# Optimization experiments

Hardware: AMD Instinct MI355X
Metric: run time of the kernel (lower is better)

## Reference

```python
import jax, jax.numpy as jnp
import numpy as np

N_NODES = 32768
N_EDGES = 131072
B = 1024          # number of drug graphs
N_SIDE = 994      # SIDER side effects
SIDE_F = 1050     # glove(300) + label(750)

GAT_DIMS = [(109, 96, 8), (768, 128, 8), (1024, 128, 8), (1024, 128, 1)]  # (in, out_per_head, heads)
LIN_DIMS = [("x5", 128, 64), ("x6", 64, 64), ("w1", 750, 750), ("w2", 750, 64),
            ("z1", 19127, 1600), ("z2", 1600, 64), ("v1", 1024, 256), ("v2", 256, 64),
            ("agg", 192, 64), ("col", 128, 64), ("s1", SIDE_F, 64), ("s2", 64, 64)]


def setup_inputs() -> dict:
    key = jax.random.key(0)
    ks = iter(jax.random.split(key, 64))
    d = {}
    d["x"] = jax.random.normal(next(ks), (N_NODES, 109), jnp.float32)
    d["edge_index"] = jax.random.randint(next(ks), (2, N_EDGES), 0, N_NODES)
    d["batch"] = jnp.arange(N_NODES) // (N_NODES // B)  # 32 atoms per graph
    d["w"] = jax.random.normal(next(ks), (B, 750), jnp.float32)
    d["z"] = jax.random.normal(next(ks), (B, 19127), jnp.float32)
    d["v"] = jax.random.normal(next(ks), (B, 1024), jnp.float32)
    d["side"] = jax.random.normal(next(ks), (N_SIDE, SIDE_F), jnp.float32)
    for i, (fi, fo, h) in enumerate(GAT_DIMS, 1):
        d[f"g{i}_W"] = jax.random.normal(next(ks), (fi, h * fo), jnp.float32) / np.sqrt(fi)
        d[f"g{i}_as"] = jax.random.normal(next(ks), (1, h, fo), jnp.float32) * 0.1
        d[f"g{i}_ad"] = jax.random.normal(next(ks), (1, h, fo), jnp.float32) * 0.1
        d[f"g{i}_b"] = jnp.zeros((h * fo,), jnp.float32)
    for name, fi, fo in LIN_DIMS:
        d[name + "_W"] = jax.random.normal(next(ks), (fi, fo), jnp.float32) / np.sqrt(fi)
        d[name + "_b"] = jnp.zeros((fo,), jnp.float32)
    return d


def _gat(x, src, dst, W, a_s, a_d, b, heads, ch):
    """PyG GATConv (eval mode): linear -> per-edge leaky_relu attention ->
    scatter-softmax over incoming edges (self-loops already in src/dst) -> scatter-sum."""
    N = x.shape[0]
    h = (x @ W).reshape(N, heads, ch)            # [N,H,C]
    al_s = (h * a_s).sum(-1)                     # [N,H]
    al_d = (h * a_d).sum(-1)                     # [N,H]
    e = jax.nn.leaky_relu(al_s[src] + al_d[dst], 0.2)  # [E,H]
    m = jax.ops.segment_max(e, dst, num_segments=N)
    p = jnp.exp(e - m[dst])
    s = jax.ops.segment_sum(p, dst, num_segments=N)
    alpha = p / s[dst]                           # softmax over neighbors of dst
    out = jax.ops.segment_sum(h[src] * alpha[:, :, None], dst, num_segments=N)
    return out.reshape(N, heads * ch) + b


def reference(x, edge_index, batch, w, z, v, side,
              g1_W, g1_as, g1_ad, g1_b, g2_W, g2_as, g2_ad, g2_b,
              g3_W, g3_as, g3_ad, g3_b, g4_W, g4_as, g4_ad, g4_b,
              x5_W, x5_b, x6_W, x6_b, w1_W, w1_b, w2_W, w2_b,
              z1_W, z1_b, z2_W, z2_b, v1_W, v1_b, v2_W, v2_b,
              agg_W, agg_b, col_W, col_b, s1_W, s1_b, s2_W, s2_b):
    relu = jax.nn.relu
    N = x.shape[0]
    nb = w.shape[0]
    loops = jnp.arange(N)
    src = jnp.concatenate([edge_index[0], loops])  # add_self_loops=True (PyG default)
    dst = jnp.concatenate([edge_index[1], loops])
    h = relu(_gat(x, src, dst, g1_W, g1_as, g1_ad, g1_b, 8, 96))
    h = relu(_gat(h, src, dst, g2_W, g2_as, g2_ad, g2_b, 8, 128))
    h = relu(_gat(h, src, dst, g3_W, g3_as, g3_ad, g3_b, 8, 128))
    h = relu(_gat(h, src, dst, g4_W, g4_as, g4_ad, g4_b, 1, 128))
    xg = jax.ops.segment_max(h, batch, num_segments=nb)           # global_max_pool
    xg = relu(relu(xg @ x5_W + x5_b) @ x6_W + x6_b)
    wv = relu(relu(w @ w1_W + w1_b) @ w2_W + w2_b)
    zv = relu(relu(z @ z1_W + z1_b) @ z2_W + z2_b)
    vv = relu(relu(v @ v1_W + v1_b) @ v2_W + v2_b)
    xwz = jnp.concatenate([xg, wv, zv], axis=1) @ agg_W + agg_b   # no activation
    drug = jnp.abs(jnp.tanh(jnp.concatenate([xwz, vv], axis=1) @ col_W + col_b))
    se = jnp.tanh(relu(side @ s1_W + s1_b) @ s2_W + s2_b)
    dn = drug / jnp.maximum(jnp.linalg.norm(drug, axis=1, keepdims=True), 1e-12)
    sn = se / jnp.maximum(jnp.linalg.norm(se, axis=1, keepdims=True), 1e-12)
    freq = 5.0 * (dn @ sn.T)
    return (freq, dn, sn)
```

## Files before the change

### kernel.cpp

```cpp
#include <hip/hip_runtime.h>
#include <math.h>
#include <float.h>

#define E0 131072
#define NN 32768
#define NB 1024
#define NSIDE 994
#define ETOT (E0 + NN)

typedef short bf16x8 __attribute__((ext_vector_type(8)));
typedef unsigned short ushort8 __attribute__((ext_vector_type(8)));
typedef float f32x4 __attribute__((ext_vector_type(4)));

__device__ inline float b2f(unsigned short u) { return __uint_as_float(((unsigned)u) << 16); }
__device__ inline unsigned short f2b(float f) {
  unsigned u = __float_as_uint(f);
  return (unsigned short)((u + 0x7fffu + ((u >> 16) & 1u)) >> 16);
}

__device__ inline void gload_lds16(const void* g, void* l) {
  __builtin_amdgcn_global_load_lds(
      (const __attribute__((address_space(1))) unsigned int*)g,
      (__attribute__((address_space(3))) unsigned int*)l, 16, 0, 0);
}

__global__ void fill_i32(int* p, int v, int n) {
  int i = blockIdx.x * blockDim.x + threadIdx.x;
  if (i < n) p[i] = v;
}

struct CDesc { const float* in; unsigned short* out; int rowsOut, Rreal, C, Cp, wg_end; };
struct CBatch { CDesc d[5]; };
__global__ void conv_batch(CBatch cb) {
  int bid = blockIdx.x;
  int di = 0;
  while (bid >= cb.d[di].wg_end) ++di;
  const CDesc& g = cb.d[di];
  int rel = bid - (di ? cb.d[di - 1].wg_end : 0);
  size_t idx = (size_t)rel * 256 + threadIdx.x;
  size_t tot = (size_t)g.rowsOut * g.Cp;
  if (idx >= tot) return;
  int r = (int)(idx / g.Cp), c = (int)(idx % g.Cp);
  g.out[idx] = (r < g.Rreal && c < g.C) ? f2b(g.in[(size_t)r * g.C + c]) : (unsigned short)0;
}

struct TDesc { const float* W; unsigned short* WT; int K, N, Kp, Npad, gx, wg_end; };
struct TBatch { TDesc d[16]; };
__global__ __launch_bounds__(256) void transpose_batch(TBatch tb) {
  __shared__ float t[32][33];
  int bid = blockIdx.x;
  int di = 0;
  while (bid >= tb.d[di].wg_end) ++di;
  const TDesc& g = tb.d[di];
  int rel = bid - (di ? tb.d[di - 1].wg_end : 0);
  int n0 = (rel % g.gx) * 32, k0 = (rel / g.gx) * 32;
  int tx = threadIdx.x & 31, ty = threadIdx.x >> 5;
  for (int r = ty; r < 32; r += 8) {
    int k = k0 + r, n = n0 + tx;
    t[r][tx] = (k < g.K && n < g.N) ? g.W[(size_t)k * g.N + n] : 0.f;
  }
  __syncthreads();
  for (int r = ty; r < 32; r += 8) {
    int n = n0 + r, k = k0 + tx;
    if (n < g.Npad && k < g.Kp)
      g.WT[(size_t)n * g.Kp + k] = (n < g.N) ? f2b(t[tx][r]) : (unsigned short)0;
  }
}

__global__ void count_deg(const int* __restrict__ ei, int* deg) {
  int e = blockIdx.x * blockDim.x + threadIdx.x;
  if (e >= ETOT) return;
  int dst = (e < E0) ? ei[E0 + e] : (e - E0);
  atomicAdd(&deg[dst], 1);
}

__global__ void scan_deg(const int* __restrict__ deg, int* rowptr, int* cursor) {
  __shared__ int part[1024];
  int tid = threadIdx.x;
  const int chunk = NN / 1024;
  int base = tid * chunk;
  int local[chunk];
  int sum = 0;
#pragma unroll
  for (int i = 0; i < chunk; ++i) { local[i] = sum; sum += deg[base + i]; }
  part[tid] = sum;
  __syncthreads();
  for (int off = 1; off < 1024; off <<= 1) {
    int t = (tid >= off) ? part[tid - off] : 0;
    __syncthreads();
    part[tid] += t;
    __syncthreads();
  }
  int offset = part[tid] - sum;
#pragma unroll
  for (int i = 0; i < chunk; ++i) {
    int v = offset + local[i];
    rowptr[base + i] = v;
    cursor[base + i] = v;
  }
  if (tid == 1023) rowptr[NN] = offset + sum;
}

__global__ void fill_csr(const int* __restrict__ ei, int* cursor,
                         int* __restrict__ srcl, int* __restrict__ pos) {
  int e = blockIdx.x * blockDim.x + threadIdx.x;
  if (e >= ETOT) return;
  int src, dst;
  if (e < E0) { src = ei[e]; dst = ei[E0 + e]; } else { src = dst = e - E0; }
  int p = atomicAdd(&cursor[dst], 1);
  srcl[p] = src;
  pos[e] = p;
}

template <int ACT, int OBF>
__global__ __launch_bounds__(256) void gemm_mfma(
    const unsigned short* __restrict__ A, const unsigned short* __restrict__ BT,
    const float* __restrict__ bias, void* __restrict__ Cp,
    int Nreal, int K, int lda, int ldb, int ldc, int gx, int zpad) {
  __shared__ unsigned short As[2][128 * 32];
  __shared__ unsigned short Bs[2][128 * 32];
  const int nwg = gridDim.x;
  const int chunk = nwg >> 3;
  const int bid = blockIdx.x;
  const int swz = (bid & 7) * chunk + (bid >> 3);
  const int bm = (swz / gx) * 128, bn = (swz % gx) * 128;
  const int tid = threadIdx.x;
  const int wv = tid >> 6, lane = tid & 63;
  const int sr = lane >> 2;
  const int sk = ((lane & 3) ^ ((lane >> 3) & 3)) * 8;
  const int r16 = lane & 15, kq = lane >> 4;
  const int slot8 = (kq ^ ((r16 >> 1) & 3)) * 8;
  const int wr = wv >> 1, wc = wv & 1;
  f32x4 acc[4][4];
#pragma unroll
  for (int i = 0; i < 4; ++i)
#pragma unroll
    for (int j = 0; j < 4; ++j) acc[i][j] = (f32x4){0.f, 0.f, 0.f, 0.f};

  const unsigned short* Abase = A + (size_t)bm * lda;
  const unsigned short* Bbase = BT + (size_t)bn * ldb;
  auto stage = [&](int buf, int k0) {
    gload_lds16(Abase + (size_t)(wv * 16 + sr) * lda + k0 + sk, &As[buf][wv * 512]);
    gload_lds16(Abase + (size_t)(64 + wv * 16 + sr) * lda + k0 + sk, &As[buf][2048 + wv * 512]);
    gload_lds16(Bbase + (size_t)(wv * 16 + sr) * ldb + k0 + sk, &Bs[buf][wv * 512]);
    gload_lds16(Bbase + (size_t)(64 + wv * 16 + sr) * ldb + k0 + sk, &Bs[buf][2048 + wv * 512]);
  };
  stage(0, 0);
  __syncthreads();
  int cur = 0;
  for (int k0 = 0; k0 < K; k0 += 32) {
    if (k0 + 32 < K) stage(cur ^ 1, k0 + 32);
    bf16x8 af[4], bfr[4];
#pragma unroll
    for (int i = 0; i < 4; ++i)
      af[i] = *(const bf16x8*)&As[cur][(wr * 64 + i * 16 + r16) * 32 + slot8];
#pragma unroll
    for (int j = 0; j < 4; ++j)
      bfr[j] = *(const bf16x8*)&Bs[cur][(wc * 64 + j * 16 + r16) * 32 + slot8];
#pragma unroll
    for (int i = 0; i < 4; ++i)
#pragma unroll
      for (int j = 0; j < 4; ++j)
        acc[i][j] = __builtin_amdgcn_mfma_f32_16x16x32_bf16(af[i], bfr[j], acc[i][j], 0, 0, 0);
    __syncthreads();
    cur ^= 1;
  }
#pragma unroll
  for (int i = 0; i < 4; ++i) {
    int row = bm + wr * 64 + i * 16 + kq * 4;
#pragma unroll
    for (int j = 0; j < 4; ++j) {
      int col = bn + wc * 64 + j * 16 + r16;
      bool real = col < Nreal;
      if (!real && !zpad) continue;
      float bv = (bias && real) ? bias[col] : 0.f;
#pragma unroll
      for (int r = 0; r < 4; ++r) {
        float v = acc[i][j][r] + bv;
        if (ACT == 1) v = v > 0.f ? v : 0.f;
        else if (ACT == 2) v = tanhf(v);
        else if (ACT == 3) v = fabsf(tanhf(v));
        if (!real) v = 0.f;
        if (OBF) ((unsigned short*)Cp)[(size_t)(row + r) * ldc + col] = f2b(v);
        else ((float*)Cp)[(size_t)(row + r) * ldc + col] = v;
      }
    }
  }
}

struct GDesc {
  const unsigned short* A; const unsigned short* BT; const float* bias; void* C;
  int Nreal, K, lda, ldb, ldc, gx, zpad, act, obf, Mreal, wg_end;
};
struct GBatch { GDesc d[5]; };
__global__ __launch_bounds__(256) void gemm_batch(GBatch gb) {
  __shared__ unsigned short As[2][128 * 32];
  __shared__ unsigned short Bs[2][128 * 32];
  int bid = blockIdx.x;
  int di = 0;
  while (bid >= gb.d[di].wg_end) ++di;
  const GDesc& g = gb.d[di];
  int rel = bid - (di ? gb.d[di - 1].wg_end : 0);
  const int bm = (rel / g.gx) * 128, bn = (rel % g.gx) * 128;
  const int tid = threadIdx.x;
  const int wv = tid >> 6, lane = tid & 63;
  const int sr = lane >> 2;
  const int sk = ((lane & 3) ^ ((lane >> 3) & 3)) * 8;
  const int r16 = lane & 15, kq = lane >> 4;
  const int slot8 = (kq ^ ((r16 >> 1) & 3)) * 8;
  const int wr = wv >> 1, wc = wv & 1;
  f32x4 acc[4][4];
#pragma unroll
  for (int i = 0; i < 4; ++i)
#pragma unroll
    for (int j = 0; j < 4; ++j) acc[i][j] = (f32x4){0.f, 0.f, 0.f, 0.f};

  const unsigned short* Abase = g.A + (size_t)bm * g.lda;
  const unsigned short* Bbase = g.BT + (size_t)bn * g.ldb;
  auto stage = [&](int buf, int k0) {
    gload_lds16(Abase + (size_t)(wv * 16 + sr) * g.lda + k0 + sk, &As[buf][wv * 512]);
    gload_lds16(Abase + (size_t)(64 + wv * 16 + sr) * g.lda + k0 + sk, &As[buf][2048 + wv * 512]);
    gload_lds16(Bbase + (size_t)(wv * 16 + sr) * g.ldb + k0 + sk, &Bs[buf][wv * 512]);
    gload_lds16(Bbase + (size_t)(64 + wv * 16 + sr) * g.ldb + k0 + sk, &Bs[buf][2048 + wv * 512]);
  };
  stage(0, 0);
  __syncthreads();
  int cur = 0;
  for (int k0 = 0; k0 < g.K; k0 += 32) {
    if (k0 + 32 < g.K) stage(cur ^ 1, k0 + 32);
    bf16x8 af[4], bfr[4];
#pragma unroll
    for (int i = 0; i < 4; ++i)
      af[i] = *(const bf16x8*)&As[cur][(wr * 64 + i * 16 + r16) * 32 + slot8];
#pragma unroll
    for (int j = 0; j < 4; ++j)
      bfr[j] = *(const bf16x8*)&Bs[cur][(wc * 64 + j * 16 + r16) * 32 + slot8];
#pragma unroll
    for (int i = 0; i < 4; ++i)
#pragma unroll
      for (int j = 0; j < 4; ++j)
        acc[i][j] = __builtin_amdgcn_mfma_f32_16x16x32_bf16(af[i], bfr[j], acc[i][j], 0, 0, 0);
    __syncthreads();
    cur ^= 1;
  }
  if (g.act == 4) {
    if (wc == 0) {
#pragma unroll
      for (int i = 0; i < 4; ++i)
#pragma unroll
        for (int r = 0; r < 4; ++r) {
          int row = bm + wr * 64 + i * 16 + kq * 4 + r;
          float vv[4];
#pragma unroll
          for (int j = 0; j < 4; ++j) vv[j] = tanhf(acc[i][j][r] + g.bias[j * 16 + r16]);
          float ss = vv[0] * vv[0] + vv[1] * vv[1] + vv[2] * vv[2] + vv[3] * vv[3];
          ss += __shfl_xor(ss, 1);
          ss += __shfl_xor(ss, 2);
          ss += __shfl_xor(ss, 4);
          ss += __shfl_xor(ss, 8);
          float inv = 1.f / fmaxf(sqrtf(ss), 1e-12f);
          if (row < g.Mreal)
#pragma unroll
            for (int j = 0; j < 4; ++j)
              ((float*)g.C)[(size_t)row * g.ldc + j * 16 + r16] = vv[j] * inv;
        }
    }
    return;
  }
#pragma unroll
  for (int i = 0; i < 4; ++i) {
    int row = bm + wr * 64 + i * 16 + kq * 4;
#pragma unroll
    for (int j = 0; j < 4; ++j) {
      int col = bn + wc * 64 + j * 16 + r16;
      bool real = col < g.Nreal;
      if (!real && !g.zpad) continue;
      float bv = (g.bias && real) ? g.bias[col] : 0.f;
#pragma unroll
      for (int r = 0; r < 4; ++r) {
        float v = acc[i][j][r] + bv;
        if (g.act == 1) v = v > 0.f ? v : 0.f;
        else if (g.act == 2) v = tanhf(v);
        else if (g.act == 3) v = fabsf(tanhf(v));
        if (!real) v = 0.f;
        if (g.obf) ((unsigned short*)g.C)[(size_t)(row + r) * g.ldc + col] = f2b(v);
        else ((float*)g.C)[(size_t)(row + r) * g.ldc + col] = v;
      }
    }
  }
}

__global__ __launch_bounds__(256) void gemm_mfma_sk(
    const unsigned short* __restrict__ A, const unsigned short* __restrict__ BT,
    unsigned short* __restrict__ PART, int lda, int ldb, int ldc) {
  __shared__ unsigned short As[128 * 32];
  __shared__ unsigned short Bs[128 * 32];
  const int bid = blockIdx.x;
  const int swz = (bid & 7) * 208 + (bid >> 3);
  const int s = swz / 104;
  const int pos = swz - s * 104;
  const int bm = (pos / 13) * 128, bn = (pos % 13) * 128;
  const int base = s * 37 + (s < 6 ? s : 6);
  const int nsteps = 37 + (s < 6 ? 1 : 0);
  const int tid = threadIdx.x;
  const int wv = tid >> 6, lane = tid & 63;
  const int sr = lane >> 2;
  const int sk = ((lane & 3) ^ ((lane >> 3) & 3)) * 8;
  const int r16 = lane & 15, kq = lane >> 4;
  const int slot8 = (kq ^ ((r16 >> 1) & 3)) * 8;
  const int wr = wv >> 1, wc = wv & 1;
  f32x4 acc[4][4];
#pragma unroll
  for (int i = 0; i < 4; ++i)
#pragma unroll
    for (int j = 0; j < 4; ++j) acc[i][j] = (f32x4){0.f, 0.f, 0.f, 0.f};

  const unsigned short* Abase = A + (size_t)bm * lda;
  const unsigned short* Bbase = BT + (size_t)bn * ldb;
  for (int ks = 0; ks < nsteps; ++ks) {
    int k0 = (base + ks) * 32;
    gload_lds16(Abase + (size_t)(wv * 16 + sr) * lda + k0 + sk, &As[wv * 512]);
    gload_lds16(Abase + (size_t)(64 + wv * 16 + sr) * lda + k0 + sk, &As[2048 + wv * 512]);
    gload_lds16(Bbase + (size_t)(wv * 16 + sr) * ldb + k0 + sk, &Bs[wv * 512]);
    gload_lds16(Bbase + (size_t)(64 + wv * 16 + sr) * ldb + k0 + sk, &Bs[2048 + wv * 512]);
    __syncthreads();
    bf16x8 af[4], bfr[4];
#pragma unroll
    for (int i = 0; i < 4; ++i)
      af[i] = *(const bf16x8*)&As[(wr * 64 + i * 16 + r16) * 32 + slot8];
#pragma unroll
    for (int j = 0; j < 4; ++j)
      bfr[j] = *(const bf16x8*)&Bs[(wc * 64 + j * 16 + r16) * 32 + slot8];
#pragma unroll
    for (int i = 0; i < 4; ++i)
#pragma unroll
      for (int j = 0; j < 4; ++j)
        acc[i][j] = __builtin_amdgcn_mfma_f32_16x16x32_bf16(af[i], bfr[j], acc[i][j], 0, 0, 0);
    __syncthreads();
  }
  unsigned short* out = PART + (size_t)s * 1024 * ldc;
#pragma unroll
  for (int i = 0; i < 4; ++i) {
    int row = bm + wr * 64 + i * 16 + kq * 4;
#pragma unroll
    for (int j = 0; j < 4; ++j) {
      int col = bn + wc * 64 + j * 16 + r16;
      if (col >= 1600) continue;
#pragma unroll
      for (int r = 0; r < 4; ++r)
        out[(size_t)(row + r) * ldc + col] = f2b(acc[i][j][r]);
    }
  }
}

__global__ void zred(const unsigned short* __restrict__ PART, const float* __restrict__ bias,
                     unsigned short* __restrict__ ZB) {
  int g = blockIdx.x * blockDim.x + threadIdx.x;
  if (g >= 1024 * 1664 / 8) return;
  size_t base = (size_t)g * 8;
  int c0 = (int)(base % 1664);
  ushort8 o;
  if (c0 >= 1600) {
#pragma unroll
    for (int t = 0; t < 8; ++t) o[t] = 0;
  } else {
    float s[8] = {0.f, 0.f, 0.f, 0.f, 0.f, 0.f, 0.f, 0.f};
#pragma unroll
    for (int k = 0; k < 16; ++k) {
      ushort8 p = *(const ushort8*)&PART[(size_t)k * 1024 * 1664 + base];
#pragma unroll
      for (int t = 0; t < 8; ++t) s[t] += b2f(p[t]);
    }
#pragma unroll
    for (int t = 0; t < 8; ++t) {
      float v = s[t] + bias[c0 + t];
      o[t] = f2b(v > 0.f ? v : 0.f);
    }
  }
  *(ushort8*)&ZB[base] = o;
}

__global__ __launch_bounds__(256) void tail_fused(
    const unsigned short* __restrict__ CAT192, const unsigned short* __restrict__ WTAGG,
    const float* __restrict__ agg_b, const unsigned short* __restrict__ CAT128,
    const unsigned short* __restrict__ WTCOL, const float* __restrict__ col_b,
    float* __restrict__ DN) {
  __shared__ unsigned short S1[128 * 32];
  __shared__ unsigned short S2[128 * 32];
  __shared__ unsigned short ACAT[128 * 128];
  const int bm = blockIdx.x * 128;
  const int tid = threadIdx.x;
  const int wv = tid >> 6, lane = tid & 63;
  const int sr = lane >> 2;
  const int sk = ((lane & 3) ^ ((lane >> 3) & 3)) * 8;
  const int r16 = lane & 15, kq = lane >> 4;
  const int slot8 = (kq ^ ((r16 >> 1) & 3)) * 8;
  const int wr = wv >> 1, wc = wv & 1;
  f32x4 acc[4][4];
#pragma unroll
  for (int i = 0; i < 4; ++i)
#pragma unroll
    for (int j = 0; j < 4; ++j) acc[i][j] = (f32x4){0.f, 0.f, 0.f, 0.f};

  const unsigned short* Abase = CAT192 + (size_t)bm * 192;
  for (int k0 = 0; k0 < 192; k0 += 32) {
    gload_lds16(Abase + (size_t)(wv * 16 + sr) * 192 + k0 + sk, &S1[wv * 512]);
    gload_lds16(Abase + (size_t)(64 + wv * 16 + sr) * 192 + k0 + sk, &S1[2048 + wv * 512]);
    gload_lds16(WTAGG + (size_t)(wv * 16 + sr) * 192 + k0 + sk, &S2[wv * 512]);
    gload_lds16(WTAGG + (size_t)(64 + wv * 16 + sr) * 192 + k0 + sk, &S2[2048 + wv * 512]);
    __syncthreads();
    bf16x8 af[4], bfr[4];
#pragma unroll
    for (int i = 0; i < 4; ++i)
      af[i] = *(const bf16x8*)&S1[(wr * 64 + i * 16 + r16) * 32 + slot8];
#pragma unroll
    for (int j = 0; j < 4; ++j)
      bfr[j] = *(const bf16x8*)&S2[(wc * 64 + j * 16 + r16) * 32 + slot8];
#pragma unroll
    for (int i = 0; i < 4; ++i)
#pragma unroll
      for (int j = 0; j < 4; ++j)
        acc[i][j] = __builtin_amdgcn_mfma_f32_16x16x32_bf16(af[i], bfr[j], acc[i][j], 0, 0, 0);
    __syncthreads();
  }
  if (wc == 0) {
#pragma unroll
    for (int i = 0; i < 4; ++i)
#pragma unroll
      for (int j = 0; j < 4; ++j) {
        int col = j * 16 + r16;
#pragma unroll
        for (int r = 0; r < 4; ++r) {
          int rl = wr * 64 + i * 16 + kq * 4 + r;
          ACAT[rl * 128 + col] = f2b(acc[i][j][r] + agg_b[col]);
        }
      }
  }
  for (int idx = tid; idx < 128 * 8; idx += 256) {
    int row = idx >> 3, c8 = (idx & 7) * 8;
    *(ushort8*)&ACAT[row * 128 + 64 + c8] =
        *(const ushort8*)&CAT128[(size_t)(bm + row) * 128 + 64 + c8];
  }
#pragma unroll
  for (int i = 0; i < 4; ++i)
#pragma unroll
    for (int j = 0; j < 4; ++j) acc[i][j] = (f32x4){0.f, 0.f, 0.f, 0.f};
  __syncthreads();

  for (int k0 = 0; k0 < 128; k0 += 32) {
    gload_lds16(WTCOL + (size_t)(wv * 16 + sr) * 128 + k0 + sk, &S1[wv * 512]);
    gload_lds16(WTCOL + (size_t)(64 + wv * 16 + sr) * 128 + k0 + sk, &S1[2048 + wv * 512]);
    __syncthreads();
    bf16x8 af[4], bfr[4];
#pragma unroll
    for (int i = 0; i < 4; ++i)
      af[i] = *(const bf16x8*)&ACAT[(wr * 64 + i * 16 + r16) * 128 + k0 + kq * 8];
#pragma unroll
    for (int j = 0; j < 4; ++j)
      bfr[j] = *(const bf16x8*)&S1[(wc * 64 + j * 16 + r16) * 32 + slot8];
#pragma unroll
    for (int i = 0; i < 4; ++i)
#pragma unroll
      for (int j = 0; j < 4; ++j)
        acc[i][j] = __builtin_amdgcn_mfma_f32_16x16x32_bf16(af[i], bfr[j], acc[i][j], 0, 0, 0);
    __syncthreads();
  }
  if (wc == 0) {
#pragma unroll
    for (int i = 0; i < 4; ++i)
#pragma unroll
      for (int r = 0; r < 4; ++r) {
        int row = bm + wr * 64 + i * 16 + kq * 4 + r;
        float vv[4];
#pragma unroll
        for (int j = 0; j < 4; ++j) vv[j] = fabsf(tanhf(acc[i][j][r] + col_b[j * 16 + r16]));
        float ss = vv[0] * vv[0] + vv[1] * vv[1] + vv[2] * vv[2] + vv[3] * vv[3];
        ss += __shfl_xor(ss, 1);
        ss += __shfl_xor(ss, 2);
        ss += __shfl_xor(ss, 4);
        ss += __shfl_xor(ss, 8);
        float inv = 1.f / fmaxf(sqrtf(ss), 1e-12f);
#pragma unroll
        for (int j = 0; j < 4; ++j)
          DN[(size_t)row * 64 + j * 16 + r16] = vv[j] * inv;
      }
  }
}

__global__ void gat_scores_bf(const unsigned short* __restrict__ hlin,
                              const float* __restrict__ a_s, const float* __restrict__ a_d,
                              float* __restrict__ als, float* __restrict__ ald,
                              int H, int C, int tot) {
  int idx = blockIdx.x * blockDim.x + threadIdx.x;
  if (idx >= tot) return;
  int n = idx / H, h = idx - n * H;
  const unsigned short* base = hlin + (size_t)n * H * C + (size_t)h * C;
  const float* as = a_s + h * C;
  const float* ad = a_d + h * C;
  float ss = 0.f, sd = 0.f;
  for (int c = 0; c < C; c += 8) {
    ushort8 v = *(const ushort8*)(base + c);
#pragma unroll
    for (int t = 0; t < 8; ++t) {
      float f = b2f(v[t]);
      ss = fmaf(f, as[c + t], ss);
      sd = fmaf(f, ad[c + t], sd);
    }
  }
  als[idx] = ss;
  ald[idx] = sd;
}

template <int H>
__global__ void edge_attn(const int* __restrict__ ei, const float* __restrict__ als,
                          const float* __restrict__ ald, const int* __restrict__ pos,
                          float* __restrict__ ebs) {
  int e = blockIdx.x * blockDim.x + threadIdx.x;
  if (e >= ETOT) return;
  int src, dst;
  if (e < E0) { src = ei[e]; dst = ei[E0 + e]; } else { src = dst = e - E0; }
  int p = pos[e];
  if (H == 8) {
    float4 s0 = *(const float4*)(als + src * 8);
    float4 s1 = *(const float4*)(als + src * 8 + 4);
    float4 d0 = *(const float4*)(ald + dst * 8);
    float4 d1 = *(const float4*)(ald + dst * 8 + 4);
    float ev[8] = {s0.x + d0.x, s0.y + d0.y, s0.z + d0.z, s0.w + d0.w,
                   s1.x + d1.x, s1.y + d1.y, s1.z + d1.z, s1.w + d1.w};
#pragma unroll
    for (int h = 0; h < 8; ++h) {
      float v = ev[h];
      v = (v >= 0.f) ? v : 0.2f * v;
      ebs[(size_t)p * 8 + h] = __expf(v);
    }
  } else {
    float v = als[src] + ald[dst];
    v = (v >= 0.f) ? v : 0.2f * v;
    ebs[p] = __expf(v);
  }
}

template <int F, int C>
__global__ __launch_bounds__(256) void gat_agg_v3(
    const int* __restrict__ rowptr, const float* __restrict__ ebs,
    const int* __restrict__ srcl, const unsigned short* __restrict__ hlin,
    const float* __restrict__ bias, unsigned short* __restrict__ out) {
  constexpr int H = F / C;
  constexpr int CPN = F / 8;
  int gidx = blockIdx.x * 256 + threadIdx.x;
  if (gidx >= NN * CPN) return;
  int node = gidx / CPN;
  int c0 = (gidx - node * CPN) * 8;
  int h = c0 / C;
  float s = 0.f;
  float acc[8] = {0.f, 0.f, 0.f, 0.f, 0.f, 0.f, 0.f, 0.f};
  int start = rowptr[node], end = rowptr[node + 1];
  for (int k = start; k < end; ++k) {
    int src = srcl[k];
    float p = ebs[(size_t)k * H + h];
    s += p;
    ushort8 hv = *(const ushort8*)(hlin + (size_t)src * F + c0);
#pragma unroll
    for (int t = 0; t < 8; ++t) acc[t] = fmaf(p, b2f(hv[t]), acc[t]);
  }
  float inv_s = 1.f / s;
  ushort8 o;
#pragma unroll
  for (int t = 0; t < 8; ++t) {
    float val = acc[t] * inv_s + bias[c0 + t];
    o[t] = f2b(val > 0.f ? val : 0.f);
  }
  *(ushort8*)(out + (size_t)node * F + c0) = o;
}

__global__ void pool_max(const unsigned short* __restrict__ xb,
                         unsigned short* __restrict__ xgb) {
  int g = blockIdx.x, c = threadIdx.x;
  const unsigned short* base = xb + (size_t)g * 32 * 128 + c;
  float m = -FLT_MAX;
#pragma unroll 8
  for (int n = 0; n < 32; ++n) m = fmaxf(m, b2f(base[n * 128]));
  xgb[g * 128 + c] = f2b(m);
}

__global__ __launch_bounds__(256) void freq_k(const float* __restrict__ dn,
                                              const float* __restrict__ sn,
                                              float* __restrict__ C, int M, int N) {
  __shared__ float As[16][64];
  __shared__ float Bs[16][65];
  int tid = threadIdx.x;
  int tx = tid & 15, ty = tid >> 4;
  int bi = blockIdx.y * 16, bj = blockIdx.x * 16;
#pragma unroll
  for (int t = 0; t < 4; ++t) {
    int idx = tid * 4 + t;
    int r = idx >> 6, c = idx & 63;
    As[r][c] = (bi + r < M) ? dn[(bi + r) * 64 + c] : 0.f;
    Bs[r][c] = (bj + r < N) ? sn[(bj + r) * 64 + c] : 0.f;
  }
  __syncthreads();
  float acc = 0.f;
#pragma unroll
  for (int k = 0; k < 64; ++k) acc = fmaf(As[ty][k], Bs[tx][k], acc);
  if (bi + ty < M && bj + tx < N) C[(size_t)(bi + ty) * N + (bj + tx)] = 5.f * acc;
}

extern "C" void kernel_launch(void* const* d_in, const int* in_sizes, int n_in,
                              void* d_out, int out_size, void* d_ws, size_t ws_size,
                              hipStream_t stream) {
  const float* x = (const float*)d_in[0];
  const int* ei = (const int*)d_in[1];
  const float* w = (const float*)d_in[3];
  const float* z = (const float*)d_in[4];
  const float* v = (const float*)d_in[5];
  const float* side = (const float*)d_in[6];
  const float* gW[4] = {(const float*)d_in[7], (const float*)d_in[11],
                        (const float*)d_in[15], (const float*)d_in[19]};
  const float* gas[4] = {(const float*)d_in[8], (const float*)d_in[12],
                         (const float*)d_in[16], (const float*)d_in[20]};
  const float* gad[4] = {(const float*)d_in[9], (const float*)d_in[13],
                         (const float*)d_in[17], (const float*)d_in[21]};
  const float* gb[4] = {(const float*)d_in[10], (const float*)d_in[14],
                        (const float*)d_in[18], (const float*)d_in[22]};
  const float* x5_W = (const float*)d_in[23]; const float* x5_b = (const float*)d_in[24];
  const float* x6_W = (const float*)d_in[25]; const float* x6_b = (const float*)d_in[26];
  const float* w1_W = (const float*)d_in[27]; const float* w1_b = (const float*)d_in[28];
  const float* w2_W = (const float*)d_in[29]; const float* w2_b = (const float*)d_in[30];
  const float* z1_W = (const float*)d_in[31]; const float* z1_b = (const float*)d_in[32];
  const float* z2_W = (const float*)d_in[33]; const float* z2_b = (const float*)d_in[34];
  const float* v1_W = (const float*)d_in[35]; const float* v1_b = (const float*)d_in[36];
  const float* v2_W = (const float*)d_in[37]; const float* v2_b = (const float*)d_in[38];
  const float* agg_W = (const float*)d_in[39]; const float* agg_b = (const float*)d_in[40];
  const float* col_W = (const float*)d_in[41]; const float* col_b = (const float*)d_in[42];
  const float* s1_W = (const float*)d_in[43]; const float* s1_b = (const float*)d_in[44];
  const float* s2_W = (const float*)d_in[45]; const float* s2_b = (const float*)d_in[46];

  char* wsb = (char*)d_ws;
  size_t off = 0;
  auto alloc = [&](size_t bytes) {
    void* p = wsb + off;
    off = (off + bytes + 255) & ~(size_t)255;
    return p;
  };
  unsigned short* HLIN = (unsigned short*)alloc((size_t)NN * 1024 * 2);
  unsigned short* XB = (unsigned short*)alloc((size_t)NN * 1024 * 2);
  unsigned short* WTZ = (unsigned short*)alloc((size_t)1664 * 19136 * 2);
  unsigned short* ZA = (unsigned short*)alloc((size_t)1024 * 19136 * 2);
  unsigned short* WT1 = (unsigned short*)alloc((size_t)768 * 128 * 2);
  unsigned short* WT2 = (unsigned short*)alloc((size_t)1024 * 768 * 2);
  unsigned short* WT3 = (unsigned short*)alloc((size_t)1024 * 1024 * 2);
  unsigned short* WT4 = (unsigned short*)alloc((size_t)128 * 1024 * 2);
  unsigned short* WTW1 = (unsigned short*)alloc((size_t)768 * 768 * 2);
  unsigned short* WTW2 = (unsigned short*)alloc((size_t)128 * 768 * 2);
  unsigned short* WTZ2 = (unsigned short*)alloc((size_t)128 * 1664 * 2);
  unsigned short* WTV1 = (unsigned short*)alloc((size_t)256 * 1024 * 2);
  unsigned short* WTV2 = (unsigned short*)alloc((size_t)128 * 256 * 2);
  unsigned short* WTX5 = (unsigned short*)alloc((size_t)128 * 128 * 2);
  unsigned short* WTX6 = (unsigned short*)alloc((size_t)128 * 64 * 2);
  unsigned short* WTAGG = (unsigned short*)alloc((size_t)128 * 192 * 2);
  unsigned short* WTCOL = (unsigned short*)alloc((size_t)128 * 128 * 2);
  unsigned short* WTS1 = (unsigned short*)alloc((size_t)128 * 1056 * 2);
  unsigned short* WTS2 = (unsigned short*)alloc((size_t)128 * 64 * 2);
  unsigned short* WB = (unsigned short*)alloc((size_t)1024 * 768 * 2);
  unsigned short* VB = (unsigned short*)alloc((size_t)1024 * 1024 * 2);
  unsigned short* SIDEB = (unsigned short*)alloc((size_t)1024 * 1056 * 2);
  unsigned short* XGB = (unsigned short*)alloc((size_t)1024 * 128 * 2);
  unsigned short* ZB = (unsigned short*)alloc((size_t)1024 * 1664 * 2);
  unsigned short* X5O = (unsigned short*)alloc((size_t)1024 * 128 * 2);
  unsigned short* WMID = (unsigned short*)alloc((size_t)1024 * 768 * 2);
  unsigned short* VMID = (unsigned short*)alloc((size_t)1024 * 256 * 2);
  unsigned short* SEMID = (unsigned short*)alloc((size_t)1024 * 128 * 2);
  unsigned short* CAT192 = (unsigned short*)alloc((size_t)1024 * 192 * 2);
  unsigned short* CAT128 = (unsigned short*)alloc((size_t)1024 * 128 * 2);
  float* EBS = (float*)alloc((size_t)ETOT * 8 * 4);
  float* ALS = (float*)alloc((size_t)NN * 8 * 4);
  float* ALD = (float*)alloc((size_t)NN * 8 * 4);
  int* DEG = (int*)alloc((size_t)NN * 4);
  int* ROWPTR = (int*)alloc((size_t)(NN + 1) * 4);
  int* CURSOR = (int*)alloc((size_t)NN * 4);
  int* SRCL = (int*)alloc((size_t)ETOT * 4);
  int* POS = (int*)alloc((size_t)ETOT * 4);
  unsigned short* PART = (unsigned short*)HLIN;

  hipLaunchKernelGGL(fill_i32, dim3((NN + 255) / 256), dim3(256), 0, stream, DEG, 0, NN);
  hipLaunchKernelGGL(count_deg, dim3((ETOT + 255) / 256), dim3(256), 0, stream, ei, DEG);
  hipLaunchKernelGGL(scan_deg, dim3(1), dim3(1024), 0, stream, DEG, ROWPTR, CURSOR);
  hipLaunchKernelGGL(fill_csr, dim3((ETOT + 255) / 256), dim3(256), 0, stream, ei, CURSOR, SRCL, POS);

  {
    TBatch tb;
    int acc_wg = 0, i = 0;
    auto add = [&](const float* W, unsigned short* WT, int K, int N, int Kp, int Npad) {
      int gx = Npad / 32, gy = Kp / 32;
      acc_wg += gx * gy;
      tb.d[i++] = {W, WT, K, N, Kp, Npad, gx, acc_wg};
    };
    add(z1_W, WTZ, 19127, 1600, 19136, 1664);
    add(gW[0], WT1, 109, 768, 128, 768);
    add(gW[1], WT2, 768, 1024, 768, 1024);
    add(gW[2], WT3, 1024, 1024, 1024, 1024);
    add(gW[3], WT4, 1024, 128, 1024, 128);
    add(w1_W, WTW1, 750, 750, 768, 768);
    add(w2_W, WTW2, 750, 64, 768, 128);
    add(z2_W, WTZ2, 1600, 64, 1664, 128);
    add(v1_W, WTV1, 1024, 256, 1024, 256);
    add(v2_W, WTV2, 256, 64, 256, 128);
    add(x5_W, WTX5, 128, 64, 128, 128);
    add(x6_W, WTX6, 64, 64, 64, 128);
    add(agg_W, WTAGG, 192, 64, 192, 128);
    add(col_W, WTCOL, 128, 64, 128, 128);
    add(s1_W, WTS1, 1050, 64, 1056, 128);
    add(s2_W, WTS2, 64, 64, 64, 128);
    hipLaunchKernelGGL(transpose_batch, dim3(acc_wg), dim3(256), 0, stream, tb);
  }

  {
    CBatch cb;
    int acc_wg = 0, i = 0;
    auto add = [&](const float* in, unsigned short* out, int rowsOut, int Rreal, int C, int Cp) {
      acc_wg += (int)(((size_t)rowsOut * Cp + 255) / 256);
      cb.d[i++] = {in, out, rowsOut, Rreal, C, Cp, acc_wg};
    };
    add(z, ZA, NB, NB, 19127, 19136);
    add(x, XB, NN, NN, 109, 128);
    add(w, WB, 1024, 1024, 750, 768);
    add(v, VB, 1024, 1024, 1024, 1024);
    add(side, SIDEB, 1024, 994, 1050, 1056);
    hipLaunchKernelGGL(conv_batch, dim3(acc_wg), dim3(256), 0, stream, cb);
  }

  auto mm = [&](const unsigned short* A, const unsigned short* BT,
                const float* bias, void* C, int M, int Npad, int Nreal, int K,
                int lda, int ldb, int ldc, int zpad) {
    int gx = Npad / 128;
    int nwg = gx * (M / 128);
    hipLaunchKernelGGL((gemm_mfma<0, 1>), dim3(nwg), dim3(256), 0, stream,
                       A, BT, bias, C, Nreal, K, lda, ldb, ldc, gx, zpad);
  };

  const int Hs[4] = {8, 8, 8, 1};
  const int Kp[4] = {128, 768, 1024, 1024};
  const unsigned short* WTs[4] = {WT1, WT2, WT3, WT4};
  const int Fs[4] = {768, 1024, 1024, 128};
  for (int l = 0; l < 4; ++l) {
    int H = Hs[l], F = Fs[l], C = F / H;
    mm(XB, WTs[l], nullptr, HLIN, NN, F, F, Kp[l], Kp[l], Kp[l], F, 0);
    int totNH = NN * H;
    hipLaunchKernelGGL(gat_scores_bf, dim3((totNH + 255) / 256), dim3(256), 0, stream,
                       HLIN, gas[l], gad[l], ALS, ALD, H, C, totNH);
    if (H == 8)
      hipLaunchKernelGGL((edge_attn<8>), dim3((ETOT + 255) / 256), dim3(256), 0, stream, ei, ALS, ALD, POS, EBS);
    else
      hipLaunchKernelGGL((edge_attn<1>), dim3((ETOT + 255) / 256), dim3(256), 0, stream, ei, ALS, ALD, POS, EBS);
    if (l == 0)
      hipLaunchKernelGGL((gat_agg_v3<768, 96>), dim3(NN * 96 / 256), dim3(256), 0, stream,
                         ROWPTR, EBS, SRCL, HLIN, gb[l], XB);
    else if (l == 3)
      hipLaunchKernelGGL((gat_agg_v3<128, 128>), dim3(NN * 16 / 256), dim3(256), 0, stream,
                         ROWPTR, EBS, SRCL, HLIN, gb[l], XB);
    else
      hipLaunchKernelGGL((gat_agg_v3<1024, 128>), dim3(NN * 128 / 256), dim3(256), 0, stream,
                         ROWPTR, EBS, SRCL, HLIN, gb[l], XB);
  }

  hipLaunchKernelGGL(pool_max, dim3(NB), dim3(128), 0, stream, XB, XGB);

  {
    GBatch b;
    int acc_wg = 0, i = 0;
    auto add = [&](const unsigned short* A, const unsigned short* BT, const float* bias,
                   void* C, int Npad, int Nreal, int K, int lda, int ldb, int ldc,
                   int zpad, int act, int obf, int Mreal) {
      int gx = Npad / 128;
      acc_wg += gx * 8;
      b.d[i++] = {A, BT, bias, C, Nreal, K, lda, ldb, ldc, gx, zpad, act, obf, Mreal, acc_wg};
    };
    add(WB, WTW1, w1_b, WMID, 768, 750, 768, 768, 768, 768, 1, 1, 1, 1024);
    add(VB, WTV1, v1_b, VMID, 256, 256, 1024, 1024, 1024, 256, 0, 1, 1, 1024);
    add(SIDEB, WTS1, s1_b, SEMID, 128, 64, 1056, 1056, 1056, 128, 1, 1, 1, 1024);
    add(XGB, WTX5, x5_b, X5O, 128, 64, 128, 128, 128, 128, 1, 1, 1, 1024);
    while (i < 5) { b.d[i] = b.d[i - 1]; b.d[i].wg_end = acc_wg; ++i; }
    hipLaunchKernelGGL(gemm_batch, dim3(acc_wg), dim3(256), 0, stream, b);
  }

  hipLaunchKernelGGL(gemm_mfma_sk, dim3(1664), dim3(256), 0, stream, ZA, WTZ, PART, 19136, 19136, 1664);
  hipLaunchKernelGGL(zred, dim3((1024 * 1664 / 8 + 255) / 256), dim3(256), 0, stream, PART, z1_b, ZB);

  float* outp = (float*)d_out;
  float* DN = outp + (size_t)NB * NSIDE;
  float* SN = DN + (size_t)NB * 64;

  {
    GBatch b;
    int acc_wg = 0, i = 0;
    auto add = [&](const unsigned short* A, const unsigned short* BT, const float* bias,
                   void* C, int Npad, int Nreal, int K, int lda, int ldb, int ldc,
                   int zpad, int act, int obf, int Mreal) {
      int gx = Npad / 128;
      acc_wg += gx * 8;
      b.d[i++] = {A, BT, bias, C, Nreal, K, lda, ldb, ldc, gx, zpad, act, obf, Mreal, acc_wg};
    };
    add(X5O, WTX6, x6_b, CAT192 + 0, 128, 64, 64, 128, 64, 192, 0, 1, 1, 1024);
    add(WMID, WTW2, w2_b, CAT192 + 64, 128, 64, 768, 768, 768, 192, 0, 1, 1, 1024);
    add(ZB, WTZ2, z2_b, CAT192 + 128, 128, 64, 1664, 1664, 1664, 192, 0, 1, 1, 1024);
    add(VMID, WTV2, v2_b, CAT128 + 64, 128, 64, 256, 256, 256, 128, 0, 1, 1, 1024);
    add(SEMID, WTS2, s2_b, SN, 128, 64, 64, 128, 64, 64, 0, 4, 0, 994);
    hipLaunchKernelGGL(gemm_batch, dim3(acc_wg), dim3(256), 0, stream, b);
  }

  hipLaunchKernelGGL(tail_fused, dim3(8), dim3(256), 0, stream,
                     CAT192, WTAGG, agg_b, CAT128, WTCOL, col_b, DN);

  hipLaunchKernelGGL(freq_k, dim3((NSIDE + 15) / 16, (NB + 15) / 16), dim3(256), 0, stream,
                     DN, SN, outp, NB, NSIDE);
}
```

Before: 1.010 ms.

## Fuse edge attention into GAT aggregation and keep split-K partials in fp32

Removes the separate edge_attn kernel and its per-edge exp buffer (EBS) plus the POS array. Attention logits are now computed inline in the aggregation loop from per-node source/destination scores. This saves four launches and the EBS write/read traffic. In exchange every thread in a head group recomputes the same exp, and gathers als[src] per edge. Separately, split-K partials for the z1 GEMM are now stored as fp32 instead of bf16. This improves accuracy but doubles the partial write/read traffic in zred.

New measurement: 986.5 us. -2.3%, faster.

```diff
diff --git a/kernel.cpp b/kernel.cpp
--- a/kernel.cpp
+++ b/kernel.cpp
@@ -101,15 +101,13 @@
   if (tid == 1023) rowptr[NN] = offset + sum;
 }
 
-__global__ void fill_csr(const int* __restrict__ ei, int* cursor,
-                         int* __restrict__ srcl, int* __restrict__ pos) {
+__global__ void fill_csr(const int* __restrict__ ei, int* cursor, int* __restrict__ srcl) {
   int e = blockIdx.x * blockDim.x + threadIdx.x;
   if (e >= ETOT) return;
   int src, dst;
   if (e < E0) { src = ei[e]; dst = ei[E0 + e]; } else { src = dst = e - E0; }
   int p = atomicAdd(&cursor[dst], 1);
   srcl[p] = src;
-  pos[e] = p;
 }
 
 template <int ACT, int OBF>
@@ -292,7 +290,7 @@
 
 __global__ __launch_bounds__(256) void gemm_mfma_sk(
     const unsigned short* __restrict__ A, const unsigned short* __restrict__ BT,
-    unsigned short* __restrict__ PART, int lda, int ldb, int ldc) {
+    float* __restrict__ PART, int lda, int ldb, int ldc) {
   __shared__ unsigned short As[128 * 32];
   __shared__ unsigned short Bs[128 * 32];
   const int bid = blockIdx.x;
@@ -338,7 +336,7 @@
         acc[i][j] = __builtin_amdgcn_mfma_f32_16x16x32_bf16(af[i], bfr[j], acc[i][j], 0, 0, 0);
     __syncthreads();
   }
-  unsigned short* out = PART + (size_t)s * 1024 * ldc;
+  float* out = PART + (size_t)s * 1024 * ldc;
 #pragma unroll
   for (int i = 0; i < 4; ++i) {
     int row = bm + wr * 64 + i * 16 + kq * 4;
@@ -348,12 +346,12 @@
       if (col >= 1600) continue;
 #pragma unroll
       for (int r = 0; r < 4; ++r)
-        out[(size_t)(row + r) * ldc + col] = f2b(acc[i][j][r]);
+        out[(size_t)(row + r) * ldc + col] = acc[i][j][r];
     }
   }
 }
 
-__global__ void zred(const unsigned short* __restrict__ PART, const float* __restrict__ bias,
+__global__ void zred(const float* __restrict__ PART, const float* __restrict__ bias,
                      unsigned short* __restrict__ ZB) {
   int g = blockIdx.x * blockDim.x + threadIdx.x;
   if (g >= 1024 * 1664 / 8) return;
@@ -367,9 +365,11 @@
     float s[8] = {0.f, 0.f, 0.f, 0.f, 0.f, 0.f, 0.f, 0.f};
 #pragma unroll
     for (int k = 0; k < 16; ++k) {
-      ushort8 p = *(const ushort8*)&PART[(size_t)k * 1024 * 1664 + base];
-#pragma unroll
-      for (int t = 0; t < 8; ++t) s[t] += b2f(p[t]);
+      const float* p = &PART[(size_t)k * 1024 * 1664 + base];
+      float4 a = *(const float4*)p;
+      float4 b = *(const float4*)(p + 4);
+      s[0] += a.x; s[1] += a.y; s[2] += a.z; s[3] += a.w;
+      s[4] += b.x; s[5] += b.y; s[6] += b.z; s[7] += b.w;
     }
 #pragma unroll
     for (int t = 0; t < 8; ++t) {
@@ -511,39 +511,11 @@
   ald[idx] = sd;
 }
 
-template <int H>
-__global__ void edge_attn(const int* __restrict__ ei, const float* __restrict__ als,
-                          const float* __restrict__ ald, const int* __restrict__ pos,
-                          float* __restrict__ ebs) {
-  int e = blockIdx.x * blockDim.x + threadIdx.x;
-  if (e >= ETOT) return;
-  int src, dst;
-  if (e < E0) { src = ei[e]; dst = ei[E0 + e]; } else { src = dst = e - E0; }
-  int p = pos[e];
-  if (H == 8) {
-    float4 s0 = *(const float4*)(als + src * 8);
-    float4 s1 = *(const float4*)(als + src * 8 + 4);
-    float4 d0 = *(const float4*)(ald + dst * 8);
-    float4 d1 = *(const float4*)(ald + dst * 8 + 4);
-    float ev[8] = {s0.x + d0.x, s0.y + d0.y, s0.z + d0.z, s0.w + d0.w,
-                   s1.x + d1.x, s1.y + d1.y, s1.z + d1.z, s1.w + d1.w};
-#pragma unroll
-    for (int h = 0; h < 8; ++h) {
-      float v = ev[h];
-      v = (v >= 0.f) ? v : 0.2f * v;
-      ebs[(size_t)p * 8 + h] = __expf(v);
-    }
-  } else {
-    float v = als[src] + ald[dst];
-    v = (v >= 0.f) ? v : 0.2f * v;
-    ebs[p] = __expf(v);
-  }
-}
-
 template <int F, int C>
-__global__ __launch_bounds__(256) void gat_agg_v3(
-    const int* __restrict__ rowptr, const float* __restrict__ ebs,
-    const int* __restrict__ srcl, const unsigned short* __restrict__ hlin,
+__global__ __launch_bounds__(256) void gat_agg_v4(
+    const int* __restrict__ rowptr, const int* __restrict__ srcl,
+    const float* __restrict__ als, const float* __restrict__ ald,
+    const unsigned short* __restrict__ hlin,
     const float* __restrict__ bias, unsigned short* __restrict__ out) {
   constexpr int H = F / C;
   constexpr int CPN = F / 8;
@@ -552,12 +524,15 @@
   int node = gidx / CPN;
   int c0 = (gidx - node * CPN) * 8;
   int h = c0 / C;
+  float aldv = ald[node * H + h];
   float s = 0.f;
   float acc[8] = {0.f, 0.f, 0.f, 0.f, 0.f, 0.f, 0.f, 0.f};
   int start = rowptr[node], end = rowptr[node + 1];
   for (int k = start; k < end; ++k) {
     int src = srcl[k];
-    float p = ebs[(size_t)k * H + h];
+    float e = als[src * H + h] + aldv;
+    e = (e >= 0.f) ? e : 0.2f * e;
+    float p = __expf(e);
     s += p;
     ushort8 hv = *(const ushort8*)(hlin + (size_t)src * F + c0);
 #pragma unroll
@@ -672,20 +647,18 @@
   unsigned short* SEMID = (unsigned short*)alloc((size_t)1024 * 128 * 2);
   unsigned short* CAT192 = (unsigned short*)alloc((size_t)1024 * 192 * 2);
   unsigned short* CAT128 = (unsigned short*)alloc((size_t)1024 * 128 * 2);
-  float* EBS = (float*)alloc((size_t)ETOT * 8 * 4);
   float* ALS = (float*)alloc((size_t)NN * 8 * 4);
   float* ALD = (float*)alloc((size_t)NN * 8 * 4);
   int* DEG = (int*)alloc((size_t)NN * 4);
   int* ROWPTR = (int*)alloc((size_t)(NN + 1) * 4);
   int* CURSOR = (int*)alloc((size_t)NN * 4);
   int* SRCL = (int*)alloc((size_t)ETOT * 4);
-  int* POS = (int*)alloc((size_t)ETOT * 4);
-  unsigned short* PART = (unsigned short*)HLIN;
+  float* PART = (float*)HLIN;
 
   hipLaunchKernelGGL(fill_i32, dim3((NN + 255) / 256), dim3(256), 0, stream, DEG, 0, NN);
   hipLaunchKernelGGL(count_deg, dim3((ETOT + 255) / 256), dim3(256), 0, stream, ei, DEG);
   hipLaunchKernelGGL(scan_deg, dim3(1), dim3(1024), 0, stream, DEG, ROWPTR, CURSOR);
-  hipLaunchKernelGGL(fill_csr, dim3((ETOT + 255) / 256), dim3(256), 0, stream, ei, CURSOR, SRCL, POS);
+  hipLaunchKernelGGL(fill_csr, dim3((ETOT + 255) / 256), dim3(256), 0, stream, ei, CURSOR, SRCL);
 
   {
     TBatch tb;
@@ -748,19 +721,15 @@
     int totNH = NN * H;
     hipLaunchKernelGGL(gat_scores_bf, dim3((totNH + 255) / 256), dim3(256), 0, stream,
                        HLIN, gas[l], gad[l], ALS, ALD, H, C, totNH);
-    if (H == 8)
-      hipLaunchKernelGGL((edge_attn<8>), dim3((ETOT + 255) / 256), dim3(256), 0, stream, ei, ALS, ALD, POS, EBS);
+    if (l == 0)
+      hipLaunchKernelGGL((gat_agg_v4<768, 96>), dim3(NN * 96 / 256), dim3(256), 0, stream,
+                         ROWPTR, SRCL, ALS, ALD, HLIN, gb[l], XB);
+    else if (l == 3)
+      hipLaunchKernelGGL((gat_agg_v4<128, 128>), dim3(NN * 16 / 256), dim3(256), 0, stream,
+                         ROWPTR, SRCL, ALS, ALD, HLIN, gb[l], XB);
     else
-      hipLaunchKernelGGL((edge_attn<1>), dim3((ETOT + 255) / 256), dim3(256), 0, stream, ei, ALS, ALD, POS, EBS);
-    if (l == 0)
-      hipLaunchKernelGGL((gat_agg_v3<768, 96>), dim3(NN * 96 / 256), dim3(256), 0, stream,
-                         ROWPTR, EBS, SRCL, HLIN, gb[l], XB);
-    else if (l == 3)
-      hipLaunchKernelGGL((gat_agg_v3<128, 128>), dim3(NN * 16 / 256), dim3(256), 0, stream,
-                         ROWPTR, EBS, SRCL, HLIN, gb[l], XB);
-    else
-      hipLaunchKernelGGL((gat_agg_v3<1024, 128>), dim3(NN * 128 / 256), dim3(256), 0, stream,
-                         ROWPTR, EBS, SRCL, HLIN, gb[l], XB);
+      hipLaunchKernelGGL((gat_agg_v4<1024, 128>), dim3(NN * 128 / 256), dim3(256), 0, stream,
+                         ROWPTR, SRCL, ALS, ALD, HLIN, gb[l], XB);
   }
 
   hipLaunchKernelGGL(pool_max, dim3(NB), dim3(128), 0, stream, XB, XGB);
```
